# Kernel tuning notes

Hardware: AMD Instinct MI355X
Metric: run time of the kernel (lower is better)

The kernel has to match this reference:

```python
import jax, jax.numpy as jnp
import numpy as np

TOPK = 50
TEMP = 5.0

def _l2norm(x):
    return x / jnp.linalg.norm(x, axis=-1, keepdims=True)

def setup_inputs() -> dict:
    key = jax.random.key(0)
    k1, k2, k3 = jax.random.split(key, 3)
    b, m, d = 32, 196, 512
    n, c = 51, 1000
    return {
        "image_features": jax.random.normal(k1, (b, d), dtype=jnp.float32),
        "local_image_features": jax.random.normal(k2, (b, m, d), dtype=jnp.float32),
        "all_text_features": jax.random.normal(k3, (n, c, d), dtype=jnp.float32),
        "logit_scale": jnp.full((1,), 4.6052, dtype=jnp.float32),  # ln(100), CLIP default
    }

def reference(image_features, local_image_features, all_text_features, logit_scale):
    # Inference path of CustomCLIP.forward (labels=None) -> get_dense_logits2
    img = _l2norm(image_features)                 # [b, d]
    loc = _l2norm(local_image_features)           # [b, m, d]
    txt = _l2norm(all_text_features)              # [n, c, d]  (n = ndisc = 51)
    mean_txt = _l2norm(txt.mean(axis=0))          # [c, d]

    base_logits = img @ mean_txt.T                # [b, c]
    w_raw = jnp.einsum('bd,bmd->bm', img, loc)    # [b, m]
    txt_cnd = jnp.transpose(txt, (1, 0, 2))       # [c, n, d]
    v = jax.nn.softmax(jnp.einsum('cd,cnd->cn', mean_txt, txt_cnd) * TEMP, axis=1)  # [c, n]

    # similarity of every patch to every description, laid out with m last for top_k
    sim = jnp.einsum('bmd,cnd->bcnm', loc, txt_cnd)        # [b, c, n, m]
    sim_topk, idx_topk = jax.lax.top_k(sim, TOPK)          # [b, c, n, k] each

    b = img.shape[0]
    # gather per-image patch weights at selected patch indices: w_raw[b, idx]
    w_topk = w_raw[jnp.arange(b)[:, None, None, None], idx_topk]   # [b, c, n, k]
    w = jax.nn.softmax(w_topk * TEMP, axis=3)               # softmax over selected patches

    bias_logits = jnp.sum(sim_topk * w * v[None, :, :, None], axis=(2, 3))  # [b, c]
    return jnp.exp(logit_scale)[0] * (base_logits + bias_logits)
```

## Files before the change

kernel.cpp:

```cpp
#include <hip/hip_runtime.h>
#include <stdint.h>

typedef __bf16  bf16x8 __attribute__((ext_vector_type(8)));
typedef float   f32x4  __attribute__((ext_vector_type(4)));
typedef short   s16x2  __attribute__((ext_vector_type(2)));
typedef unsigned short u16;

#define TEMP 5.0f

__device__ inline float wsum(float v){
  #pragma unroll
  for (int off=32; off; off>>=1) v += __shfl_xor(v, off, 64);
  return v;
}
__device__ inline float wmax(float v){
  #pragma unroll
  for (int off=32; off; off>>=1) v = fmaxf(v, __shfl_xor(v, off, 64));
  return v;
}
__device__ inline u16 f2bf(float f){
  unsigned u = __float_as_uint(f);
  u = u + 0x7fffu + ((u>>16)&1u);
  return (u16)(u>>16);
}
__device__ inline float bfl(unsigned u){ return __uint_as_float(u<<16); }
__device__ inline float bfh(unsigned u){ return __uint_as_float(u & 0xffff0000u); }

__device__ inline s16x2 as_s16x2(int v){ union{int i; s16x2 v;} u; u.i=v; return u.v; }

__device__ inline s16x2 pkmin2(s16x2 a, s16x2 b){
  s16x2 r; r.x = a.x < b.x ? a.x : b.x; r.y = a.y < b.y ? a.y : b.y; return r;
}
__device__ inline s16x2 pkmax2(s16x2 a, s16x2 b){
  s16x2 r; r.x = a.x > b.x ? a.x : b.x; r.y = a.y > b.y ? a.y : b.y; return r;
}

#if __has_builtin(__builtin_amdgcn_mov_dpp)
__device__ inline int dxor1(int v){ return __builtin_amdgcn_mov_dpp(v, 0xB1, 0xF, 0xF, true); }
__device__ inline int dxor2(int v){ return __builtin_amdgcn_mov_dpp(v, 0x4E, 0xF, 0xF, true); }
#else
__device__ inline int dxor1(int v){ return __shfl_xor(v, 1, 64); }
__device__ inline int dxor2(int v){ return __shfl_xor(v, 2, 64); }
#endif

#if __has_builtin(__builtin_amdgcn_permlane16_swap)
__device__ inline int x16sum_i(int c){
  auto p = __builtin_amdgcn_permlane16_swap((unsigned)c, (unsigned)c, false, false);
  return (int)p[0] + (int)p[1];
}
__device__ inline int x16min_i(int c){
  auto p = __builtin_amdgcn_permlane16_swap((unsigned)c, (unsigned)c, false, false);
  return min((int)p[0], (int)p[1]);
}
__device__ inline int x16max_i(int c){
  auto p = __builtin_amdgcn_permlane16_swap((unsigned)c, (unsigned)c, false, false);
  return max((int)p[0], (int)p[1]);
}
__device__ inline float x16sum_f(float v){
  auto p = __builtin_amdgcn_permlane16_swap(__float_as_uint(v), __float_as_uint(v), false, false);
  return __uint_as_float(p[0]) + __uint_as_float(p[1]);
}
#else
__device__ inline int   x16sum_i(int c){ return c + __shfl_xor(c, 16, 64); }
__device__ inline int   x16min_i(int c){ return min(c, __shfl_xor(c, 16, 64)); }
__device__ inline int   x16max_i(int c){ return max(c, __shfl_xor(c, 16, 64)); }
__device__ inline float x16sum_f(float v){ return v + __shfl_xor(v, 16, 64); }
#endif

__device__ inline int ssum8_i(int c){ c += dxor1(c); c += dxor2(c); return x16sum_i(c); }
__device__ inline int smin8_i(int c){ c = min(c, dxor1(c)); c = min(c, dxor2(c)); return x16min_i(c); }
__device__ inline int smax8_i(int c){ c = max(c, dxor1(c)); c = max(c, dxor2(c)); return x16max_i(c); }
__device__ inline float ssum8_f(float v){
  v += __int_as_float(dxor1(__float_as_int(v)));
  v += __int_as_float(dxor2(__float_as_int(v)));
  return x16sum_f(v);
}

__device__ inline void cp16(void* lds_uniform, const void* g){
  __builtin_amdgcn_global_load_lds(
    (const __attribute__((address_space(1))) unsigned int*)g,
    (__attribute__((address_space(3))) unsigned int*)lds_uniform, 16, 0, 0);
}

__global__ void k_img(const float* __restrict__ X, float* __restrict__ imgn){
  int b = blockIdx.x, lane = threadIdx.x;
  const float* src = X + (size_t)b*512 + lane*8;
  float4 a = *(const float4*)src;
  float4 c = *(const float4*)(src+4);
  float ss = a.x*a.x+a.y*a.y+a.z*a.z+a.w*a.w + c.x*c.x+c.y*c.y+c.z*c.z+c.w*c.w;
  ss = wsum(ss);
  float inv = 1.0f/sqrtf(ss);
  float* dst = imgn + (size_t)b*512 + lane*8;
  float4 o0 = {a.x*inv,a.y*inv,a.z*inv,a.w*inv};
  float4 o1 = {c.x*inv,c.y*inv,c.z*inv,c.w*inv};
  *(float4*)dst = o0; *(float4*)(dst+4) = o1;
}

__global__ void k_txt(const float* __restrict__ X, u16* __restrict__ TXT, float* __restrict__ invn){
  int cn = blockIdx.x, lane = threadIdx.x;
  int kc = lane>>2, kk8 = (lane&3)*8;
  size_t dstE = ((size_t)kc*51008 + cn)*32 + kk8;
  if (cn >= 51000){
    uint4 z = {0,0,0,0};
    *(uint4*)(TXT + dstE) = z;
    return;
  }
  int c = cn/51, n = cn - c*51;
  const float* src = X + ((size_t)n*1000 + c)*512 + lane*8;
  float4 a = *(const float4*)src;
  float4 d = *(const float4*)(src+4);
  float ss = a.x*a.x+a.y*a.y+a.z*a.z+a.w*a.w + d.x*d.x+d.y*d.y+d.z*d.z+d.w*d.w;
  ss = wsum(ss);
  float inv = 1.0f/sqrtf(ss);
  u16 h0=f2bf(a.x*inv),h1=f2bf(a.y*inv),h2=f2bf(a.z*inv),h3=f2bf(a.w*inv);
  u16 h4=f2bf(d.x*inv),h5=f2bf(d.y*inv),h6=f2bf(d.z*inv),h7=f2bf(d.w*inv);
  uint4 o;
  o.x = (unsigned)h0 | ((unsigned)h1<<16);
  o.y = (unsigned)h2 | ((unsigned)h3<<16);
  o.z = (unsigned)h4 | ((unsigned)h5<<16);
  o.w = (unsigned)h6 | ((unsigned)h7<<16);
  *(uint4*)(TXT + dstE) = o;
  if (lane==0) invn[(size_t)n*1000 + c] = inv;
}

__global__ void k_mean(const float* __restrict__ X, const float* __restrict__ invn, float* __restrict__ MT){
  int c = blockIdx.x, tid = threadIdx.x, lane = tid&63, wv = tid>>6;
  __shared__ float sinv[51];
  __shared__ float red[4];
  if (tid < 51) sinv[tid] = invn[(size_t)tid*1000 + c];
  __syncthreads();
  int d0 = tid*2;
  float sx=0.f, sy=0.f;
  for (int n=0;n<51;++n){
    const float2 x = *(const float2*)(X + ((size_t)n*1000 + c)*512 + d0);
    float iv = sinv[n];
    sx += x.x*iv; sy += x.y*iv;
  }
  float ss = sx*sx + sy*sy;
  ss = wsum(ss);
  if (lane==0) red[wv] = ss;
  __syncthreads();
  float tot = red[0]+red[1]+red[2]+red[3];
  float inv = 1.0f/sqrtf(tot);
  float2 o = {sx*inv, sy*inv};
  *(float2*)(MT + (size_t)c*512 + d0) = o;
}

__global__ void k_v(const u16* __restrict__ TXT, const float* __restrict__ MT, float* __restrict__ vbuf){
  int c = blockIdx.x, lane = threadIdx.x;
  __shared__ float lg[51];
  const float* mp = MT + (size_t)c*512 + lane*8;
  float4 m0 = *(const float4*)mp;
  float4 m1 = *(const float4*)(mp+4);
  int kc = lane>>2, kk8 = (lane&3)*8;
  for (int n=0;n<51;++n){
    size_t e = ((size_t)kc*51008 + (size_t)(c*51+n))*32 + kk8;
    uint4 q = *(const uint4*)(TXT + e);
    float d = bfl(q.x)*m0.x + bfh(q.x)*m0.y + bfl(q.y)*m0.z + bfh(q.y)*m0.w
            + bfl(q.z)*m1.x + bfh(q.z)*m1.y + bfl(q.w)*m1.z + bfh(q.w)*m1.w;
    d = wsum(d);
    if (lane==0) lg[n] = d;
  }
  __syncthreads();
  float val = (lane<51) ? lg[lane] : -1e30f;
  float mx = wmax(val);
  float e = (lane<51) ? expf(TEMP*(val-mx)) : 0.f;
  float s = wsum(e);
  if (lane<51) vbuf[(size_t)c*51 + lane] = e/s;
}

__global__ void k_base(const float* __restrict__ imgn, const float* __restrict__ MT, float* __restrict__ bias){
  int c = blockIdx.x, lane = threadIdx.x;
  const float* mp = MT + (size_t)c*512 + lane*8;
  float4 m0 = *(const float4*)mp;
  float4 m1 = *(const float4*)(mp+4);
  for (int b=0;b<32;++b){
    const float* ip = imgn + (size_t)b*512 + lane*8;
    float4 i0 = *(const float4*)ip;
    float4 i1 = *(const float4*)(ip+4);
    float d = i0.x*m0.x+i0.y*m0.y+i0.z*m0.z+i0.w*m0.w
            + i1.x*m1.x+i1.y*m1.y+i1.z*m1.z+i1.w*m1.w;
    d = wsum(d);
    if (lane==0) bias[(size_t)b*1000 + c] = d;
  }
}

__global__ void k_loc(const float* __restrict__ L, const float* __restrict__ imgn,
                      u16* __restrict__ LOC, float* __restrict__ ewg){
  int m = blockIdx.x, b = blockIdx.y, lane = threadIdx.x;
  size_t dstE = ((size_t)(b*16 + (lane>>2))*224 + m)*32 + (lane&3)*8;
  if (m >= 196){
    uint4 z = {0,0,0,0};
    *(uint4*)(LOC + dstE) = z;
    if (lane==0) ewg[(size_t)b*224 + m] = 0.f;
    return;
  }
  const float* src = L + ((size_t)b*196 + m)*512 + lane*8;
  float4 a = *(const float4*)src;
  float4 d = *(const float4*)(src+4);
  const float* ip = imgn + (size_t)b*512 + lane*8;
  float4 i0 = *(const float4*)ip;
  float4 i1 = *(const float4*)(ip+4);
  float ss = a.x*a.x+a.y*a.y+a.z*a.z+a.w*a.w + d.x*d.x+d.y*d.y+d.z*d.z+d.w*d.w;
  float ws = a.x*i0.x+a.y*i0.y+a.z*i0.z+a.w*i0.w + d.x*i1.x+d.y*i1.y+d.z*i1.z+d.w*i1.w;
  ss = wsum(ss); ws = wsum(ws);
  float inv = 1.0f/sqrtf(ss);
  u16 h0=f2bf(a.x*inv),h1=f2bf(a.y*inv),h2=f2bf(a.z*inv),h3=f2bf(a.w*inv);
  u16 h4=f2bf(d.x*inv),h5=f2bf(d.y*inv),h6=f2bf(d.z*inv),h7=f2bf(d.w*inv);
  uint4 o;
  o.x = (unsigned)h0 | ((unsigned)h1<<16);
  o.y = (unsigned)h2 | ((unsigned)h3<<16);
  o.z = (unsigned)h4 | ((unsigned)h5<<16);
  o.w = (unsigned)h6 | ((unsigned)h7<<16);
  *(uint4*)(LOC + dstE) = o;
  if (lane==0) ewg[(size_t)b*224 + m] = expf(TEMP * ws * inv);
}

__global__ __launch_bounds__(512,8) void k_main(const u16* __restrict__ TXT, const u16* __restrict__ LOC,
                                                const float* __restrict__ ewg, const float* __restrict__ vbuf,
                                                float* __restrict__ bias){
  __shared__ __align__(16) char smem[30592];
  const int tid = threadIdx.x, lane = tid & 63, wv = tid >> 6;
  const int quad = lane >> 4, l16 = lane & 15;
  const int wm = wv >> 1, wn = wv & 1;
  const int NT = (wm == 3) ? 2 : 4;
  const int lsw = lane ^ ((lane>>3)&3);
  const int qsw = (quad ^ ((l16>>1)&3)) * 16;
  const int sub = (lane & 3) | ((lane >> 2) & 4);
  const int col = ((lane >> 2) & 3) | ((lane >> 3) & 4);

  int id = blockIdx.x, b, cnt_;
  if (id < 24576){
    int g = id >> 10, r = id & 1023;
    b = r >> 5;  cnt_ = (g << 5) + (r & 31);
  } else {
    int r = id - 24576;
    b = r / 29;  cnt_ = 768 + r % 29;
  }
  const int cn0 = cnt_ * 64;

  float* ewl = (float*)(smem + 29696);
  if (tid < 224) ewl[tid] = ewg[(size_t)b*224 + tid];

  const f32x4 zero = {0.f,0.f,0.f,0.f};
  f32x4 acc[4][2];
  #pragma unroll
  for (int t=0;t<4;++t){ acc[t][0]=zero; acc[t][1]=zero; }

  const u16* Abase = LOC + (size_t)(b*16)*224*32;
  char* Albd0 = smem;
  char* Albd1 = smem + 14336;

  auto stageA = [&](int kc, char* dst){
    const char* src = (const char*)(Abase + (size_t)kc*224*32);
    #pragma unroll
    for (int j=0;j<2;++j){
      int ch0 = j*512 + wv*64;
      if (ch0 < 896)
        cp16(dst + (size_t)ch0*16, src + (size_t)(ch0 + lsw)*16);
    }
  };
  struct B2 { bf16x8 x, y; };
  auto loadB = [&](int kc)->B2{
    B2 r;
    size_t e = ((size_t)kc*51008 + (size_t)(cn0 + 32*wn + l16))*32 + quad*8;
    r.x = *(const bf16x8*)(TXT + e);
    r.y = *(const bf16x8*)(TXT + e + 16*32);
    return r;
  };
  auto domfma = [&](const char* Ab, B2 bb){
    #pragma unroll
    for (int t=0;t<4;++t){
      if (t < NT){
        bf16x8 af = *(const bf16x8*)(Ab + (size_t)(((4*wm + t)*16 + l16)*64) + qsw);
        acc[t][0] = __builtin_amdgcn_mfma_f32_16x16x32_bf16(af, bb.x, acc[t][0], 0,0,0);
        acc[t][1] = __builtin_amdgcn_mfma_f32_16x16x32_bf16(af, bb.y, acc[t][1], 0,0,0);
      }
    }
  };

  stageA(0, Albd0);
  __syncthreads();

  for (int kc = 0; kc < 16; ++kc){
    char* cur = (kc & 1) ? Albd1 : Albd0;
    char* nxt = (kc & 1) ? Albd0 : Albd1;
    B2 bb = loadB(kc);
    if (kc < 15) stageA(kc+1, nxt);
    domfma(cur, bb);
    __syncthreads();
  }

  const float KSC = 15360.0f;
  {
    #pragma unroll
    for (int n=0;n<2;++n){
      unsigned* wr = (unsigned*)(void*)smem + (size_t)((2*wn + n)*1856) + l16*116 + quad*2;
      #pragma unroll
      for (int t=0;t<4;++t){
        if (t < NT){
          int a0 = (int)(acc[t][n][0]*KSC), a1 = (int)(acc[t][n][1]*KSC);
          int a2 = (int)(acc[t][n][2]*KSC), a3 = (int)(acc[t][n][3]*KSC);
          uint2 o; o.x = (unsigned)((a0 & 0xffff) | (a1<<16)); o.y = (unsigned)((a2 & 0xffff) | (a3<<16));
          *(uint2*)(wr + (4*wm + t)*8) = o;
        }
      }
    }
  }
  __syncthreads();

  int kk[7][2];
  {
    const unsigned* rd = (const unsigned*)(void*)smem + (size_t)((wv>>1)*1856) + ((wv&1)*8 + col)*116 + sub*14;
    #pragma unroll
    for (int j=0;j<7;++j){
      uint2 q = *(const uint2*)(rd + 2*j);
      kk[j][0] = (int)q.x;
      kk[j][1] = (int)q.y;
    }
  }
  const int PKPK = (int)0xC180C180;
  if (sub == 7){
    #pragma unroll
    for (int j=0;j<7;++j){ kk[j][0] = PKPK; kk[j][1] = PKPK; }
  }

  s16x2 vmn = as_s16x2(kk[0][0]), vmx = vmn;
  #pragma unroll
  for (int j=0;j<7;++j){
    #pragma unroll
    for (int i=0;i<2;++i){
      vmn = pkmin2(vmn, as_s16x2(kk[j][i]));
      vmx = pkmax2(vmx, as_s16x2(kk[j][i]));
    }
  }
  int kmn = min((int)vmn.x, (int)vmn.y);
  int kmx = max((int)vmx.x, (int)vmx.y);
  if (sub == 7){ kmn = 32000; kmx = -32000; }
  kmn = smin8_i(kmn);
  kmx = smax8_i(kmx);
  int lo = kmn - 1, hi = kmx + 1;

  auto count_ge = [&](int tm)->int{
    int t1 = tm - 1;
    s16x2 tmv = as_s16x2((t1 & 0xffff) | (t1 << 16));
    s16x2 ca = {0,0};
    #pragma unroll
    for (int j=0;j<7;++j){
      ca = ca + ((tmv - as_s16x2(kk[j][0])) >> 15);
      ca = ca + ((tmv - as_s16x2(kk[j][1])) >> 15);
    }
    return ssum8_i(-((int)ca.x + (int)ca.y));
  };

  int samp = (kk[3][0]<<16)>>16;
  if (sub == 7) samp = -32768;
  int mx1 = smax8_i(samp);
  int m2  = smax8_i(samp == mx1 ? -32768 : samp);
  int tm0 = min(hi - 1, max(lo + 1, m2));
  int c0  = count_ge(tm0);

  float flo = 146.0f, fhi = -50.0f;
  int side;
  if (c0 >= 50){ lo = tm0; flo = (float)(c0 - 50); side = 1; }
  else         { hi = tm0; fhi = (float)(c0 - 50); side = -1; }
  bool done = (c0 == 50) || ((hi - lo) <= 1);

  #pragma unroll 1
  for (int it = 0; it < 12; ++it){
    if (__all(done)) break;
    float fr = flo * __builtin_amdgcn_rcpf(flo - fhi);
    fr = fminf(fmaxf(fr, 0.04f), 0.96f);
    int tm = lo + (int)(fr * (float)(hi - lo));
    tm = (tm <= lo) ? (lo + 1) : ((tm >= hi) ? (hi - 1) : tm);

    int c = count_ge(tm);
    bool ge = (c >= 50);
    if (!done){
      if (ge){ fhi = (side==1)  ? fhi*0.5f : fhi; flo = (float)(c-50); lo = tm; side = 1; }
      else   { flo = (side==-1) ? flo*0.5f : flo; fhi = (float)(c-50); hi = tm; side = -1; }
    }
    done = done || (c == 50) || ((hi - lo) <= 1);
  }
  const int thr = lo;

  float num = 0.f, den = 0.f;
  #pragma unroll
  for (int j=0;j<7;++j){
    float2 e0 = *(const float2*)(ewl + 28*sub + 4*j);
    float2 e1 = *(const float2*)(ewl + 28*sub + 4*j + 2);
    int a0 = (kk[j][0]<<16)>>16, a1 = kk[j][0]>>16;
    int a2 = (kk[j][1]<<16)>>16, a3 = kk[j][1]>>16;
    if (a0 >= thr){ num = fmaf((float)a0, e0.x, num); den += e0.x; }
    if (a1 >= thr){ num = fmaf((float)a1, e0.y, num); den += e0.y; }
    if (a2 >= thr){ num = fmaf((float)a2, e1.x, num); den += e1.x; }
    if (a3 >= thr){ num = fmaf((float)a3, e1.y, num); den += e1.y; }
  }
  num = ssum8_f(num);
  den = ssum8_f(den);

  int cn = cn0 + (wv>>1)*16 + (wv&1)*8 + col;
  if (sub == 0 && cn < 51000){
    int c = cn/51;
    atomicAdd(bias + (size_t)b*1000 + c, vbuf[cn]*(num/(den*KSC)));
  }
}

__global__ void k_out(const float* __restrict__ bias, const float* __restrict__ ls, float* __restrict__ out){
  int i = blockIdx.x*256 + threadIdx.x;
  if (i < 32000){
    float sc = expf(ls[0]);
    out[i] = sc * bias[i];
  }
}

extern "C" void kernel_launch(void* const* d_in, const int* in_sizes, int n_in,
                              void* d_out, int out_size, void* d_ws, size_t ws_size,
                              hipStream_t stream) {
  const float* img = (const float*)d_in[0];
  const float* loc = (const float*)d_in[1];
  const float* txt = (const float*)d_in[2];
  const float* ls  = (const float*)d_in[3];
  char* ws = (char*)d_ws;
  float* imgn = (float*)(ws + 0);
  float* MT   = (float*)(ws + 65536);
  float* invn = (float*)(ws + 2113536);
  float* vbuf = (float*)(ws + 2317568);
  float* ewg  = (float*)(ws + 2521600);
  float* bias = (float*)(ws + 2550272);
  u16*   TXT  = (u16*)  (ws + 2678272);
  u16*   LOC  = (u16*)  (ws + 54910464);

  k_img <<<dim3(32),      dim3(64),  0, stream>>>(img, imgn);
  k_txt <<<dim3(51008),   dim3(64),  0, stream>>>(txt, TXT, invn);
  k_mean<<<dim3(1000),    dim3(256), 0, stream>>>(txt, invn, MT);
  k_v   <<<dim3(1000),    dim3(64),  0, stream>>>(TXT, MT, vbuf);
  k_base<<<dim3(1000),    dim3(64),  0, stream>>>(imgn, MT, bias);
  k_loc <<<dim3(224,32),  dim3(64),  0, stream>>>(loc, imgn, LOC, ewg);
  k_main<<<dim3(25504),   dim3(512), 0, stream>>>(TXT, LOC, ewg, vbuf, bias);
  k_out <<<dim3(125),     dim3(256), 0, stream>>>(bias, ls, (float*)d_out);
}
```

Measured before the change: 1.007 ms.

## Halve k_main block to 4 waves with 7 M-tiles each and 4-lane top-k

The main fused GEMM+top-k kernel now runs 256 threads (4 waves) per block instead of 512. Each wave computes 7 M-tiles, 112 patches, instead of up to 4, so every B fragment loaded from global memory is reused across more MFMAs. The top-k threshold search now splits each column's 224 patch scores across 4 lanes (one per quad) instead of 8 sub-lanes, and reduces with permlane16/32 swaps instead of DPP. The initial lower bound is a fixed constant instead of a computed minimum. The trade-off is more accumulator and kk registers per thread (launch bounds 256,5), lower occupancy and more serial work per lane in the counting loop.

```diff
diff --git a/kernel.cpp b/kernel.cpp
--- a/kernel.cpp
+++ b/kernel.cpp
@@ -28,30 +28,15 @@
 
 __device__ inline s16x2 as_s16x2(int v){ union{int i; s16x2 v;} u; u.i=v; return u.v; }
 
-__device__ inline s16x2 pkmin2(s16x2 a, s16x2 b){
-  s16x2 r; r.x = a.x < b.x ? a.x : b.x; r.y = a.y < b.y ? a.y : b.y; return r;
-}
 __device__ inline s16x2 pkmax2(s16x2 a, s16x2 b){
   s16x2 r; r.x = a.x > b.x ? a.x : b.x; r.y = a.y > b.y ? a.y : b.y; return r;
 }
 
-#if __has_builtin(__builtin_amdgcn_mov_dpp)
-__device__ inline int dxor1(int v){ return __builtin_amdgcn_mov_dpp(v, 0xB1, 0xF, 0xF, true); }
-__device__ inline int dxor2(int v){ return __builtin_amdgcn_mov_dpp(v, 0x4E, 0xF, 0xF, true); }
-#else
-__device__ inline int dxor1(int v){ return __shfl_xor(v, 1, 64); }
-__device__ inline int dxor2(int v){ return __shfl_xor(v, 2, 64); }
-#endif
-
-#if __has_builtin(__builtin_amdgcn_permlane16_swap)
+#if __has_builtin(__builtin_amdgcn_permlane16_swap) && __has_builtin(__builtin_amdgcn_permlane32_swap)
 __device__ inline int x16sum_i(int c){
   auto p = __builtin_amdgcn_permlane16_swap((unsigned)c, (unsigned)c, false, false);
   return (int)p[0] + (int)p[1];
 }
-__device__ inline int x16min_i(int c){
-  auto p = __builtin_amdgcn_permlane16_swap((unsigned)c, (unsigned)c, false, false);
-  return min((int)p[0], (int)p[1]);
-}
 __device__ inline int x16max_i(int c){
   auto p = __builtin_amdgcn_permlane16_swap((unsigned)c, (unsigned)c, false, false);
   return max((int)p[0], (int)p[1]);
@@ -60,21 +45,30 @@
   auto p = __builtin_amdgcn_permlane16_swap(__float_as_uint(v), __float_as_uint(v), false, false);
   return __uint_as_float(p[0]) + __uint_as_float(p[1]);
 }
+__device__ inline int x32sum_i(int c){
+  auto p = __builtin_amdgcn_permlane32_swap((unsigned)c, (unsigned)c, false, false);
+  return (int)p[0] + (int)p[1];
+}
+__device__ inline int x32max_i(int c){
+  auto p = __builtin_amdgcn_permlane32_swap((unsigned)c, (unsigned)c, false, false);
+  return max((int)p[0], (int)p[1]);
+}
+__device__ inline float x32sum_f(float v){
+  auto p = __builtin_amdgcn_permlane32_swap(__float_as_uint(v), __float_as_uint(v), false, false);
+  return __uint_as_float(p[0]) + __uint_as_float(p[1]);
+}
 #else
 __device__ inline int   x16sum_i(int c){ return c + __shfl_xor(c, 16, 64); }
-__device__ inline int   x16min_i(int c){ return min(c, __shfl_xor(c, 16, 64)); }
 __device__ inline int   x16max_i(int c){ return max(c, __shfl_xor(c, 16, 64)); }
 __device__ inline float x16sum_f(float v){ return v + __shfl_xor(v, 16, 64); }
+__device__ inline int   x32sum_i(int c){ return c + __shfl_xor(c, 32, 64); }
+__device__ inline int   x32max_i(int c){ return max(c, __shfl_xor(c, 32, 64)); }
+__device__ inline float x32sum_f(float v){ return v + __shfl_xor(v, 32, 64); }
 #endif
 
-__device__ inline int ssum8_i(int c){ c += dxor1(c); c += dxor2(c); return x16sum_i(c); }
-__device__ inline int smin8_i(int c){ c = min(c, dxor1(c)); c = min(c, dxor2(c)); return x16min_i(c); }
-__device__ inline int smax8_i(int c){ c = max(c, dxor1(c)); c = max(c, dxor2(c)); return x16max_i(c); }
-__device__ inline float ssum8_f(float v){
-  v += __int_as_float(dxor1(__float_as_int(v)));
-  v += __int_as_float(dxor2(__float_as_int(v)));
-  return x16sum_f(v);
-}
+__device__ inline int   qsum4_i(int c){ return x32sum_i(x16sum_i(c)); }
+__device__ inline int   qmax4_i(int c){ return x32max_i(x16max_i(c)); }
+__device__ inline float qsum4_f(float v){ return x32sum_f(x16sum_f(v)); }
 
 __device__ inline void cp16(void* lds_uniform, const void* g){
   __builtin_amdgcn_global_load_lds(
@@ -216,18 +210,15 @@
   if (lane==0) ewg[(size_t)b*224 + m] = expf(TEMP * ws * inv);
 }
 
-__global__ __launch_bounds__(512,8) void k_main(const u16* __restrict__ TXT, const u16* __restrict__ LOC,
+__global__ __launch_bounds__(256,5) void k_main(const u16* __restrict__ TXT, const u16* __restrict__ LOC,
                                                 const float* __restrict__ ewg, const float* __restrict__ vbuf,
                                                 float* __restrict__ bias){
   __shared__ __align__(16) char smem[30592];
   const int tid = threadIdx.x, lane = tid & 63, wv = tid >> 6;
   const int quad = lane >> 4, l16 = lane & 15;
-  const int wm = wv >> 1, wn = wv & 1;
-  const int NT = (wm == 3) ? 2 : 4;
+  const int ms = wv >> 1, ns = wv & 1;
   const int lsw = lane ^ ((lane>>3)&3);
   const int qsw = (quad ^ ((l16>>1)&3)) * 16;
-  const int sub = (lane & 3) | ((lane >> 2) & 4);
-  const int col = ((lane >> 2) & 3) | ((lane >> 3) & 4);
 
   int id = blockIdx.x, b, cnt_;
   if (id < 24576){
@@ -243,9 +234,9 @@
   if (tid < 224) ewl[tid] = ewg[(size_t)b*224 + tid];
 
   const f32x4 zero = {0.f,0.f,0.f,0.f};
-  f32x4 acc[4][2];
+  f32x4 acc[7][2];
   #pragma unroll
-  for (int t=0;t<4;++t){ acc[t][0]=zero; acc[t][1]=zero; }
+  for (int t=0;t<7;++t){ acc[t][0]=zero; acc[t][1]=zero; }
 
   const u16* Abase = LOC + (size_t)(b*16)*224*32;
   char* Albd0 = smem;
@@ -254,8 +245,8 @@
   auto stageA = [&](int kc, char* dst){
     const char* src = (const char*)(Abase + (size_t)kc*224*32);
     #pragma unroll
-    for (int j=0;j<2;++j){
-      int ch0 = j*512 + wv*64;
+    for (int j=0;j<4;++j){
+      int ch0 = j*256 + wv*64;
       if (ch0 < 896)
         cp16(dst + (size_t)ch0*16, src + (size_t)(ch0 + lsw)*16);
     }
@@ -263,19 +254,17 @@
   struct B2 { bf16x8 x, y; };
   auto loadB = [&](int kc)->B2{
     B2 r;
-    size_t e = ((size_t)kc*51008 + (size_t)(cn0 + 32*wn + l16))*32 + quad*8;
+    size_t e = ((size_t)kc*51008 + (size_t)(cn0 + 32*ns + l16))*32 + quad*8;
     r.x = *(const bf16x8*)(TXT + e);
     r.y = *(const bf16x8*)(TXT + e + 16*32);
     return r;
   };
   auto domfma = [&](const char* Ab, B2 bb){
     #pragma unroll
-    for (int t=0;t<4;++t){
-      if (t < NT){
-        bf16x8 af = *(const bf16x8*)(Ab + (size_t)(((4*wm + t)*16 + l16)*64) + qsw);
-        acc[t][0] = __builtin_amdgcn_mfma_f32_16x16x32_bf16(af, bb.x, acc[t][0], 0,0,0);
-        acc[t][1] = __builtin_amdgcn_mfma_f32_16x16x32_bf16(af, bb.y, acc[t][1], 0,0,0);
-      }
+    for (int t=0;t<7;++t){
+      bf16x8 af = *(const bf16x8*)(Ab + (size_t)((112*ms + 16*t + l16)*64) + qsw);
+      acc[t][0] = __builtin_amdgcn_mfma_f32_16x16x32_bf16(af, bb.x, acc[t][0], 0,0,0);
+      acc[t][1] = __builtin_amdgcn_mfma_f32_16x16x32_bf16(af, bb.y, acc[t][1], 0,0,0);
     }
   };
 
@@ -294,69 +283,60 @@
   const float KSC = 15360.0f;
   {
     #pragma unroll
-    for (int n=0;n<2;++n){
-      unsigned* wr = (unsigned*)(void*)smem + (size_t)((2*wn + n)*1856) + l16*116 + quad*2;
+    for (int z=0;z<2;++z){
+      unsigned* wr = (unsigned*)(void*)smem + (size_t)((2*ns + z)*1856) + l16*116 + quad*2;
       #pragma unroll
-      for (int t=0;t<4;++t){
-        if (t < NT){
-          int a0 = (int)(acc[t][n][0]*KSC), a1 = (int)(acc[t][n][1]*KSC);
-          int a2 = (int)(acc[t][n][2]*KSC), a3 = (int)(acc[t][n][3]*KSC);
-          uint2 o; o.x = (unsigned)((a0 & 0xffff) | (a1<<16)); o.y = (unsigned)((a2 & 0xffff) | (a3<<16));
-          *(uint2*)(wr + (4*wm + t)*8) = o;
-        }
+      for (int t=0;t<7;++t){
+        int a0 = (int)(acc[t][z][0]*KSC), a1 = (int)(acc[t][z][1]*KSC);
+        int a2 = (int)(acc[t][z][2]*KSC), a3 = (int)(acc[t][z][3]*KSC);
+        uint2 o; o.x = (unsigned)((a0 & 0xffff) | (a1<<16)); o.y = (unsigned)((a2 & 0xffff) | (a3<<16));
+        *(uint2*)(wr + (7*ms + t)*8) = o;
       }
     }
   }
   __syncthreads();
 
-  int kk[7][2];
+  int kk[14][2];
   {
-    const unsigned* rd = (const unsigned*)(void*)smem + (size_t)((wv>>1)*1856) + ((wv&1)*8 + col)*116 + sub*14;
-    #pragma unroll
-    for (int j=0;j<7;++j){
+    const unsigned* rd = (const unsigned*)(void*)smem + (size_t)(wv*1856) + l16*116 + quad*28;
+    #pragma unroll
+    for (int j=0;j<14;++j){
       uint2 q = *(const uint2*)(rd + 2*j);
       kk[j][0] = (int)q.x;
       kk[j][1] = (int)q.y;
     }
   }
   const int PKPK = (int)0xC180C180;
-  if (sub == 7){
-    #pragma unroll
-    for (int j=0;j<7;++j){ kk[j][0] = PKPK; kk[j][1] = PKPK; }
-  }
-
-  s16x2 vmn = as_s16x2(kk[0][0]), vmx = vmn;
+  if (quad == 3){
+    #pragma unroll
+    for (int j=7;j<14;++j){ kk[j][0] = PKPK; kk[j][1] = PKPK; }
+  }
+
+  s16x2 vmx = as_s16x2(kk[0][0]);
   #pragma unroll
-  for (int j=0;j<7;++j){
-    #pragma unroll
-    for (int i=0;i<2;++i){
-      vmn = pkmin2(vmn, as_s16x2(kk[j][i]));
-      vmx = pkmax2(vmx, as_s16x2(kk[j][i]));
-    }
-  }
-  int kmn = min((int)vmn.x, (int)vmn.y);
+  for (int j=0;j<14;++j){
+    vmx = pkmax2(vmx, as_s16x2(kk[j][0]));
+    vmx = pkmax2(vmx, as_s16x2(kk[j][1]));
+  }
   int kmx = max((int)vmx.x, (int)vmx.y);
-  if (sub == 7){ kmn = 32000; kmx = -32000; }
-  kmn = smin8_i(kmn);
-  kmx = smax8_i(kmx);
-  int lo = kmn - 1, hi = kmx + 1;
+  kmx = qmax4_i(kmx);
+  int lo = -15600, hi = kmx + 1;
 
   auto count_ge = [&](int tm)->int{
     int t1 = tm - 1;
     s16x2 tmv = as_s16x2((t1 & 0xffff) | (t1 << 16));
     s16x2 ca = {0,0};
     #pragma unroll
-    for (int j=0;j<7;++j){
+    for (int j=0;j<14;++j){
       ca = ca + ((tmv - as_s16x2(kk[j][0])) >> 15);
       ca = ca + ((tmv - as_s16x2(kk[j][1])) >> 15);
     }
-    return ssum8_i(-((int)ca.x + (int)ca.y));
+    return qsum4_i(-((int)ca.x + (int)ca.y));
   };
 
   int samp = (kk[3][0]<<16)>>16;
-  if (sub == 7) samp = -32768;
-  int mx1 = smax8_i(samp);
-  int m2  = smax8_i(samp == mx1 ? -32768 : samp);
+  int mx1 = qmax4_i(samp);
+  int m2  = qmax4_i(samp == mx1 ? -32768 : samp);
   int tm0 = min(hi - 1, max(lo + 1, m2));
   int c0  = count_ge(tm0);
 
@@ -386,21 +366,20 @@
 
   float num = 0.f, den = 0.f;
   #pragma unroll
-  for (int j=0;j<7;++j){
-    float2 e0 = *(const float2*)(ewl + 28*sub + 4*j);
-    float2 e1 = *(const float2*)(ewl + 28*sub + 4*j + 2);
-    int a0 = (kk[j][0]<<16)>>16, a1 = kk[j][0]>>16;
-    int a2 = (kk[j][1]<<16)>>16, a3 = kk[j][1]>>16;
-    if (a0 >= thr){ num = fmaf((float)a0, e0.x, num); den += e0.x; }
-    if (a1 >= thr){ num = fmaf((float)a1, e0.y, num); den += e0.y; }
-    if (a2 >= thr){ num = fmaf((float)a2, e1.x, num); den += e1.x; }
-    if (a3 >= thr){ num = fmaf((float)a3, e1.y, num); den += e1.y; }
-  }
-  num = ssum8_f(num);
-  den = ssum8_f(den);
-
-  int cn = cn0 + (wv>>1)*16 + (wv&1)*8 + col;
-  if (sub == 0 && cn < 51000){
+  for (int j=0;j<14;++j){
+    #pragma unroll
+    for (int i=0;i<2;++i){
+      float2 e = *(const float2*)(ewl + 56*quad + 4*j + 2*i);
+      int a0 = (kk[j][i]<<16)>>16, a1 = kk[j][i]>>16;
+      if (a0 >= thr){ num = fmaf((float)a0, e.x, num); den += e.x; }
+      if (a1 >= thr){ num = fmaf((float)a1, e.y, num); den += e.y; }
+    }
+  }
+  num = qsum4_f(num);
+  den = qsum4_f(den);
+
+  int cn = cn0 + 16*wv + l16;
+  if (quad == 0 && cn < 51000){
     int c = cn/51;
     atomicAdd(bias + (size_t)b*1000 + c, vbuf[cn]*(num/(den*KSC)));
   }
@@ -437,6 +416,6 @@
   k_v   <<<dim3(1000),    dim3(64),  0, stream>>>(TXT, MT, vbuf);
   k_base<<<dim3(1000),    dim3(64),  0, stream>>>(imgn, MT, bias);
   k_loc <<<dim3(224,32),  dim3(64),  0, stream>>>(loc, imgn, LOC, ewg);
-  k_main<<<dim3(25504),   dim3(512), 0, stream>>>(TXT, LOC, ewg, vbuf, bias);
+  k_main<<<dim3(25504),   dim3(256), 0, stream>>>(TXT, LOC, ewg, vbuf, bias);
   k_out <<<dim3(125),     dim3(256), 0, stream>>>(bias, ls, (float*)d_out);
 }
```

Measured after the change: 965.0 us. 4.1% less time.
